# Optimization experiments

Measured on AMD Instinct MI355X. Metric: run time of the kernel, lower is better.

Reference implementation:

```python
import jax, jax.numpy as jnp
import numpy as np

GRID_SHAPE = (128, 128, 128, 8)
N_POINTS = 2_000_000


def setup_inputs() -> dict:
    key = jax.random.key(0)
    k1, k2 = jax.random.split(key)
    coords = jax.random.uniform(k1, (N_POINTS, 3), dtype=jnp.float32)
    grid = jax.random.normal(k2, GRID_SHAPE, dtype=jnp.float32)
    bbox_min = jnp.zeros((3,), dtype=jnp.float32)
    bbox_max = jnp.ones((3,), dtype=jnp.float32)
    return {"coords": coords, "grid": grid, "bbox_min": bbox_min, "bbox_max": bbox_max}


def reference(coords, grid, bbox_min, bbox_max):
    # coords: [N, 3]; grid: [X, Y, Z, C]
    eps = 1e-06
    coords = coords[:, :3]
    scale = jnp.maximum(bbox_max - bbox_min, eps)
    normalized = jnp.clip((coords - bbox_min) / scale, 0.0, 1.0)
    grid_size = jnp.asarray(grid.shape[:3], dtype=jnp.int64)  # [3]
    pos = normalized * (grid_size.astype(coords.dtype) - 1.0)  # [N, 3]
    idx0 = jnp.floor(pos).astype(jnp.int64)                    # [N, 3]
    idx1 = jnp.minimum(idx0 + 1, grid_size - 1)                # [N, 3]
    weight = jnp.clip(pos - idx0.astype(coords.dtype), 0.0, 1.0)  # [N, 3]

    x0, y0, z0 = idx0[:, 0], idx0[:, 1], idx0[:, 2]
    x1, y1, z1 = idx1[:, 0], idx1[:, 1], idx1[:, 2]
    wx, wy, wz = weight[:, 0:1], weight[:, 1:2], weight[:, 2:3]  # each [N, 1]

    c000 = grid[x0, y0, z0]
    c100 = grid[x1, y0, z0]
    c010 = grid[x0, y1, z0]
    c110 = grid[x1, y1, z0]
    c001 = grid[x0, y0, z1]
    c101 = grid[x1, y0, z1]
    c011 = grid[x0, y1, z1]
    c111 = grid[x1, y1, z1]

    c00 = c000 * (1.0 - wx) + c100 * wx
    c01 = c001 * (1.0 - wx) + c101 * wx
    c10 = c010 * (1.0 - wx) + c110 * wx
    c11 = c011 * (1.0 - wx) + c111 * wx
    c0 = c00 * (1.0 - wy) + c10 * wy
    c1 = c01 * (1.0 - wy) + c11 * wy
    return c0 * (1.0 - wz) + c1 * wz  # [N, C]
```

## Files before the change

kernel.cpp:

```cpp
#include <hip/hip_runtime.h>


#define GS    128
#define NBX   32
#define NB2   2048
#define CAP1  65536
#define CAP2  1280
#define K_PTS 1024

__device__ __forceinline__ void cell_of(
    float cx, float cy, float cz,
    float b0x, float b0y, float b0z,
    float sx, float sy, float sz,
    int& x0, int& y0, int& z0)
{
    float nx = fminf(fmaxf((cx - b0x) / sx, 0.0f), 1.0f);
    float ny = fminf(fmaxf((cy - b0y) / sy, 0.0f), 1.0f);
    float nz = fminf(fmaxf((cz - b0z) / sz, 0.0f), 1.0f);
    x0 = (int)(nx * (float)(GS - 1));
    y0 = (int)(ny * (float)(GS - 1));
    z0 = (int)(nz * (float)(GS - 1));
}

__global__ __launch_bounds__(256) void k_init(
    unsigned* __restrict__ cursor32, unsigned* __restrict__ cursor2048)
{
    int i = blockIdx.x * 256 + threadIdx.x;
    if (i < NBX) cursor32[i] = (unsigned)i * CAP1;
    if (i < NB2) cursor2048[i] = (unsigned)i * CAP2;
}

__global__ __launch_bounds__(256) void k_scatter1(
    const float* __restrict__ coords,
    const float* __restrict__ bbox_min,
    const float* __restrict__ bbox_max,
    unsigned* __restrict__ cursor32,
    float4* __restrict__ recs1, int n)
{
    __shared__ float4 srec[K_PTS];
    __shared__ unsigned char sbkt[K_PTS];
    __shared__ unsigned cnt[NBX], lbase[NBX], gbase[NBX];

    int t = threadIdx.x;
    if (t < NBX) cnt[t] = 0;
    __syncthreads();

    float b0x = bbox_min[0];
    float sx  = fmaxf(bbox_max[0] - b0x, 1e-6f);
    long long base = (long long)blockIdx.x * K_PTS;
    int m = (int)min((long long)K_PTS, (long long)n - base);

    float cx[4], cy[4], cz[4];
    int bb[4]; unsigned rr[4];
    int j0 = 4 * t;
    if (j0 + 3 < m) {
        const float4* c4 = (const float4*)coords + (size_t)blockIdx.x * 768 + 3 * t;
        float4 f0 = c4[0], f1 = c4[1], f2 = c4[2];
        cx[0] = f0.x; cy[0] = f0.y; cz[0] = f0.z;
        cx[1] = f0.w; cy[1] = f1.x; cz[1] = f1.y;
        cx[2] = f1.z; cy[2] = f1.w; cz[2] = f2.x;
        cx[3] = f2.y; cy[3] = f2.z; cz[3] = f2.w;
    } else {
#pragma unroll
        for (int p = 0; p < 4; ++p) {
            int j = j0 + p;
            if (j < m) {
                long long i = base + j;
                cx[p] = coords[3 * i]; cy[p] = coords[3 * i + 1]; cz[p] = coords[3 * i + 2];
            }
        }
    }
#pragma unroll
    for (int p = 0; p < 4; ++p) {
        int j = j0 + p;
        if (j < m) {
            float nx = fminf(fmaxf((cx[p] - b0x) / sx, 0.0f), 1.0f);
            bb[p] = ((int)(nx * (float)(GS - 1))) >> 2;
            rr[p] = atomicAdd(&cnt[bb[p]], 1u);
        }
    }
    __syncthreads();

    if (t == 0) {
        unsigned acc = 0;
        for (int j = 0; j < NBX; ++j) { lbase[j] = acc; acc += cnt[j]; }
    }
    if (t < NBX && cnt[t]) gbase[t] = atomicAdd(&cursor32[t], cnt[t]);
    __syncthreads();

#pragma unroll
    for (int p = 0; p < 4; ++p) {
        int j = j0 + p;
        if (j < m) {
            unsigned slot = lbase[bb[p]] + rr[p];
            float4 r; r.x = cx[p]; r.y = cy[p]; r.z = cz[p];
            r.w = __uint_as_float((unsigned)(base + j));
            srec[slot] = r;
            sbkt[slot] = (unsigned char)bb[p];
        }
    }
    __syncthreads();

#pragma unroll
    for (int k = 0; k < 4; ++k) {
        int j = k * 256 + t;
        if (j < m) {
            int b = sbkt[j];
            unsigned d = gbase[b] + (unsigned)j - lbase[b];
            if (d < (unsigned)(b + 1) * CAP1) recs1[d] = srec[j];
        }
    }
}

__global__ __launch_bounds__(256) void k_scatter2(
    const float4* __restrict__ recs1,
    const float* __restrict__ bbox_min,
    const float* __restrict__ bbox_max,
    const unsigned* __restrict__ cursor32_final,
    unsigned* __restrict__ cursor2048,
    float4* __restrict__ recs2)
{
    __shared__ float4 srec[K_PTS];
    __shared__ unsigned char sbkt[K_PTS];
    __shared__ unsigned cnt[64], lbase[64], gbase[64];

    int s = blockIdx.x >> 6;
    int c = blockIdx.x & 63;
    unsigned fill = cursor32_final[s] - (unsigned)s * CAP1;
    if (fill > CAP1) fill = CAP1;
    unsigned off = (unsigned)c * 1024;
    if (off >= fill) return;
    int m = (int)min(1024u, fill - off);

    int t = threadIdx.x;
    if (t < 64) cnt[t] = 0;
    __syncthreads();

    float b0x = bbox_min[0], b0y = bbox_min[1], b0z = bbox_min[2];
    float sx = fmaxf(bbox_max[0] - b0x, 1e-6f);
    float sy = fmaxf(bbox_max[1] - b0y, 1e-6f);
    float sz = fmaxf(bbox_max[2] - b0z, 1e-6f);
    long long base = (long long)s * CAP1 + off;

    float4 rc[4]; int bb[4]; unsigned rr[4];
#pragma unroll
    for (int k = 0; k < 4; ++k) {
        int j = k * 256 + t;
        if (j < m) {
            rc[k] = recs1[base + j];
            int x0, y0, z0;
            cell_of(rc[k].x, rc[k].y, rc[k].z, b0x, b0y, b0z, sx, sy, sz, x0, y0, z0);
            bb[k] = ((y0 >> 2) << 1) | (z0 >> 6);
            rr[k] = atomicAdd(&cnt[bb[k]], 1u);
        }
    }
    __syncthreads();

    if (t == 0) {
        unsigned acc = 0;
        for (int j = 0; j < 64; ++j) { lbase[j] = acc; acc += cnt[j]; }
    }
    if (t < 64 && cnt[t]) gbase[t] = atomicAdd(&cursor2048[s * 64 + t], cnt[t]);
    __syncthreads();

#pragma unroll
    for (int k = 0; k < 4; ++k) {
        int j = k * 256 + t;
        if (j < m) {
            unsigned slot = lbase[bb[k]] + rr[k];
            srec[slot] = rc[k];
            sbkt[slot] = (unsigned char)bb[k];
        }
    }
    __syncthreads();

#pragma unroll
    for (int k = 0; k < 4; ++k) {
        int j = k * 256 + t;
        if (j < m) {
            int lb = sbkt[j];
            unsigned g = (unsigned)s * 64 + lb;
            unsigned d = gbase[lb] + (unsigned)j - lbase[lb];
            if (d < (g + 1) * CAP2) recs2[d] = srec[j];
        }
    }
}

#define LDS_CELLS (5 * 5 * 65)
__global__ __launch_bounds__(256) void k_interp_staged(
    const float4* __restrict__ recs2,
    const unsigned* __restrict__ cursor2048_final,
    const float* __restrict__ grid,
    const float* __restrict__ bbox_min,
    const float* __restrict__ bbox_max,
    float4* __restrict__ out4)
{
    __shared__ float4 tile[LDS_CELLS * 2];

    int ob = blockIdx.x;
    int b  = (ob & 7) * 256 + (ob >> 3);

    unsigned s0 = (unsigned)b * CAP2;
    unsigned e  = cursor2048_final[b];
    unsigned cap_end = s0 + CAP2;
    if (e > cap_end) e = cap_end;
    if (e <= s0) return;

    int xs = b >> 6, ys = (b >> 1) & 31, zh = b & 1;
    int t = threadIdx.x;

    const float4* g4 = (const float4*)grid;
    for (int k = t; k < LDS_CELLS * 2; k += 256) {
        int c  = k >> 1, half = k & 1;
        int lx = c / 325;
        int r2 = c - lx * 325;
        int ly = r2 / 65;
        int lz = r2 - ly * 65;
        int gx = min(xs * 4 + lx, GS - 1);
        int gy = min(ys * 4 + ly, GS - 1);
        int gz = min(zh * 64 + lz, GS - 1);
        tile[k] = g4[(((gx * GS) + gy) * GS + gz) * 2 + half];
    }
    __syncthreads();

    const float eps = 1e-6f;
    float b0x = bbox_min[0], b0y = bbox_min[1], b0z = bbox_min[2];
    float sx = fmaxf(bbox_max[0] - b0x, eps);
    float sy = fmaxf(bbox_max[1] - b0y, eps);
    float sz = fmaxf(bbox_max[2] - b0z, eps);

    int pair = t >> 1, half = t & 1;

    for (unsigned cb = s0; cb < e; cb += 128) {
        unsigned j = cb + pair;
        if (j >= e) continue;
        float4 rec = recs2[j];
        unsigned orig = __float_as_uint(rec.w);

        float nx = fminf(fmaxf((rec.x - b0x) / sx, 0.0f), 1.0f);
        float ny = fminf(fmaxf((rec.y - b0y) / sy, 0.0f), 1.0f);
        float nz = fminf(fmaxf((rec.z - b0z) / sz, 0.0f), 1.0f);
        float px = nx * (float)(GS - 1);
        float py = ny * (float)(GS - 1);
        float pz = nz * (float)(GS - 1);
        int x0 = (int)px, y0 = (int)py, z0 = (int)pz;
        int x1 = min(x0 + 1, GS - 1);
        int y1 = min(y0 + 1, GS - 1);
        int z1 = min(z0 + 1, GS - 1);
        float wx = fminf(fmaxf(px - (float)x0, 0.0f), 1.0f);
        float wy = fminf(fmaxf(py - (float)y0, 0.0f), 1.0f);
        float wz = fminf(fmaxf(pz - (float)z0, 0.0f), 1.0f);

        int lx0 = x0 - xs * 4, lx1 = x1 - xs * 4;
        int ly0 = y0 - ys * 4, ly1 = y1 - ys * 4;
        int lz0 = z0 - zh * 64, lz1 = z1 - zh * 64;

        int c000 = ((lx0 * 5 + ly0) * 65 + lz0) * 2 + half;
        int c100 = ((lx1 * 5 + ly0) * 65 + lz0) * 2 + half;
        int c010 = ((lx0 * 5 + ly1) * 65 + lz0) * 2 + half;
        int c110 = ((lx1 * 5 + ly1) * 65 + lz0) * 2 + half;
        int c001 = ((lx0 * 5 + ly0) * 65 + lz1) * 2 + half;
        int c101 = ((lx1 * 5 + ly0) * 65 + lz1) * 2 + half;
        int c011 = ((lx0 * 5 + ly1) * 65 + lz1) * 2 + half;
        int c111 = ((lx1 * 5 + ly1) * 65 + lz1) * 2 + half;

        float ux = 1.0f - wx, uy = 1.0f - wy, uz = 1.0f - wz;
        float w000 = ux*uy*uz, w100 = wx*uy*uz, w010 = ux*wy*uz, w110 = wx*wy*uz;
        float w001 = ux*uy*wz, w101 = wx*uy*wz, w011 = ux*wy*wz, w111 = wx*wy*wz;

        float4 A = tile[c000], B = tile[c100], C = tile[c010], D = tile[c110];
        float4 E = tile[c001], F = tile[c101], H = tile[c011], Kk = tile[c111];

        float4 o;
        o.x = A.x*w000 + B.x*w100 + C.x*w010 + D.x*w110 + E.x*w001 + F.x*w101 + H.x*w011 + Kk.x*w111;
        o.y = A.y*w000 + B.y*w100 + C.y*w010 + D.y*w110 + E.y*w001 + F.y*w101 + H.y*w011 + Kk.y*w111;
        o.z = A.z*w000 + B.z*w100 + C.z*w010 + D.z*w110 + E.z*w001 + F.z*w101 + H.z*w011 + Kk.z*w111;
        o.w = A.w*w000 + B.w*w100 + C.w*w010 + D.w*w110 + E.w*w001 + F.w*w101 + H.w*w011 + Kk.w*w111;

        out4[(long long)orig * 2 + half] = o;
    }
}

__global__ __launch_bounds__(256) void trilerp_direct(
    const float* __restrict__ coords,
    const float* __restrict__ grid,
    const float* __restrict__ bbox_min,
    const float* __restrict__ bbox_max,
    float* __restrict__ out, int n)
{
    int i = blockIdx.x * blockDim.x + threadIdx.x;
    if (i >= n) return;
    const float eps = 1e-6f;
    float b0x = bbox_min[0], b0y = bbox_min[1], b0z = bbox_min[2];
    float sx = fmaxf(bbox_max[0] - b0x, eps);
    float sy = fmaxf(bbox_max[1] - b0y, eps);
    float sz = fmaxf(bbox_max[2] - b0z, eps);
    float nx = fminf(fmaxf((coords[3*i] - b0x) / sx, 0.0f), 1.0f);
    float ny = fminf(fmaxf((coords[3*i+1] - b0y) / sy, 0.0f), 1.0f);
    float nz = fminf(fmaxf((coords[3*i+2] - b0z) / sz, 0.0f), 1.0f);
    float px = nx * (float)(GS - 1), py = ny * (float)(GS - 1), pz = nz * (float)(GS - 1);
    int x0 = (int)px, y0 = (int)py, z0 = (int)pz;
    int x1 = min(x0 + 1, GS - 1), y1 = min(y0 + 1, GS - 1), z1 = min(z0 + 1, GS - 1);
    float wx = fminf(fmaxf(px - (float)x0, 0.0f), 1.0f);
    float wy = fminf(fmaxf(py - (float)y0, 0.0f), 1.0f);
    float wz = fminf(fmaxf(pz - (float)z0, 0.0f), 1.0f);
    float ux = 1.0f - wx, uy = 1.0f - wy, uz = 1.0f - wz;
    float w000 = ux*uy*uz, w100 = wx*uy*uz, w010 = ux*wy*uz, w110 = wx*wy*uz;
    float w001 = ux*uy*wz, w101 = wx*uy*wz, w011 = ux*wy*wz, w111 = wx*wy*wz;
    const float4* g4 = (const float4*)grid;
    int bx0 = x0 * GS, bx1 = x1 * GS;
    int p000 = ((bx0 + y0) * GS + z0) * 2, p100 = ((bx1 + y0) * GS + z0) * 2;
    int p010 = ((bx0 + y1) * GS + z0) * 2, p110 = ((bx1 + y1) * GS + z0) * 2;
    int p001 = ((bx0 + y0) * GS + z1) * 2, p101 = ((bx1 + y0) * GS + z1) * 2;
    int p011 = ((bx0 + y1) * GS + z1) * 2, p111 = ((bx1 + y1) * GS + z1) * 2;
    float4 a0 = g4[p000], a1 = g4[p000+1], b0 = g4[p100], b1 = g4[p100+1];
    float4 c0 = g4[p010], c1 = g4[p010+1], d0 = g4[p110], d1 = g4[p110+1];
    float4 e0 = g4[p001], e1 = g4[p001+1], f0 = g4[p101], f1 = g4[p101+1];
    float4 h0 = g4[p011], h1 = g4[p011+1], k0 = g4[p111], k1 = g4[p111+1];
    float4 o0, o1;
    o0.x = a0.x*w000 + b0.x*w100 + c0.x*w010 + d0.x*w110 + e0.x*w001 + f0.x*w101 + h0.x*w011 + k0.x*w111;
    o0.y = a0.y*w000 + b0.y*w100 + c0.y*w010 + d0.y*w110 + e0.y*w001 + f0.y*w101 + h0.y*w011 + k0.y*w111;
    o0.z = a0.z*w000 + b0.z*w100 + c0.z*w010 + d0.z*w110 + e0.z*w001 + f0.z*w101 + h0.z*w011 + k0.z*w111;
    o0.w = a0.w*w000 + b0.w*w100 + c0.w*w010 + d0.w*w110 + e0.w*w001 + f0.w*w101 + h0.w*w011 + k0.w*w111;
    o1.x = a1.x*w000 + b1.x*w100 + c1.x*w010 + d1.x*w110 + e1.x*w001 + f1.x*w101 + h1.x*w011 + k1.x*w111;
    o1.y = a1.y*w000 + b1.y*w100 + c1.y*w010 + d1.y*w110 + e1.y*w001 + f1.y*w101 + h1.y*w011 + k1.y*w111;
    o1.z = a1.z*w000 + b1.z*w100 + c1.z*w010 + d1.z*w110 + e1.z*w001 + f1.z*w101 + h1.z*w011 + k1.z*w111;
    o1.w = a1.w*w000 + b1.w*w100 + c1.w*w010 + d1.w*w110 + e1.w*w001 + f1.w*w101 + h1.w*w011 + k1.w*w111;
    float4* outp = (float4*)out;
    outp[(long long)i * 2 + 0] = o0;
    outp[(long long)i * 2 + 1] = o1;
}

extern "C" void kernel_launch(void* const* d_in, const int* in_sizes, int n_in,
                              void* d_out, int out_size, void* d_ws, size_t ws_size,
                              hipStream_t stream) {
    const float* coords   = (const float*)d_in[0];
    const float* grid     = (const float*)d_in[1];
    const float* bbox_min = (const float*)d_in[2];
    const float* bbox_max = (const float*)d_in[3];
    float* out = (float*)d_out;

    int n = in_sizes[0] / 3;

    size_t cur32_off = 0;
    size_t cur2_off  = 256;
    size_t recs1_off = 16384;
    size_t recs2_off = recs1_off + (size_t)NBX * CAP1 * 16;
    size_t needed    = recs2_off + (size_t)NB2 * CAP2 * 16;

    int nb_sort = (n + K_PTS - 1) / K_PTS;
    int nb_dir  = (n + 255) / 256;

    if (ws_size >= needed) {
        unsigned* cur32 = (unsigned*)((char*)d_ws + cur32_off);
        unsigned* cur2  = (unsigned*)((char*)d_ws + cur2_off);
        float4*   recs1 = (float4*)((char*)d_ws + recs1_off);
        float4*   recs2 = (float4*)((char*)d_ws + recs2_off);

        k_init    <<<8, 256, 0, stream>>>(cur32, cur2);
        k_scatter1<<<nb_sort, 256, 0, stream>>>(coords, bbox_min, bbox_max, cur32, recs1, n);
        k_scatter2<<<NBX * 64, 256, 0, stream>>>(recs1, bbox_min, bbox_max, cur32, cur2, recs2);
        k_interp_staged<<<NB2, 256, 0, stream>>>(recs2, cur2, grid, bbox_min, bbox_max,
                                                 (float4*)out);
    } else {
        trilerp_direct<<<nb_dir, 256, 0, stream>>>(coords, grid, bbox_min, bbox_max, out, n);
    }
}
```

Baseline: 98.24 us.

## Halve z extent of interpolation tiles, double bucket count, stage records in LDS

Second-level buckets now split z into quarters (32 cells) instead of halves, which doubles the bucket count to 4096 and shrinks the per-bucket grid tile to 5x5x33 cells. The interpolation kernel now runs 512 threads per block and first copies its bucket's point records into shared memory before working on them. The smaller tile means less redundant grid halo loading per point and more, smaller blocks to spread across the GPU. The risk is that the per-bucket capacity of 704 is tight against the expected ~488 points per bucket, so a heavily filled bucket could overflow and drop points.

```diff
diff --git a/kernel.cpp b/kernel.cpp
--- a/kernel.cpp
+++ b/kernel.cpp
@@ -3,10 +3,11 @@
 
 #define GS    128
 #define NBX   32
-#define NB2   2048
+#define NB2   4096
 #define CAP1  65536
-#define CAP2  1280
+#define CAP2  704
 #define K_PTS 1024
+#define HCELLS (5 * 5 * 33)
 
 __device__ __forceinline__ void cell_of(
     float cx, float cy, float cz,
@@ -23,11 +24,11 @@
 }
 
 __global__ __launch_bounds__(256) void k_init(
-    unsigned* __restrict__ cursor32, unsigned* __restrict__ cursor2048)
+    unsigned* __restrict__ cursor32, unsigned* __restrict__ cursor4096)
 {
     int i = blockIdx.x * 256 + threadIdx.x;
     if (i < NBX) cursor32[i] = (unsigned)i * CAP1;
-    if (i < NB2) cursor2048[i] = (unsigned)i * CAP2;
+    if (i < NB2) cursor4096[i] = (unsigned)i * CAP2;
 }
 
 __global__ __launch_bounds__(256) void k_scatter1(
@@ -117,12 +118,12 @@
     const float* __restrict__ bbox_min,
     const float* __restrict__ bbox_max,
     const unsigned* __restrict__ cursor32_final,
-    unsigned* __restrict__ cursor2048,
+    unsigned* __restrict__ cursor4096,
     float4* __restrict__ recs2)
 {
     __shared__ float4 srec[K_PTS];
     __shared__ unsigned char sbkt[K_PTS];
-    __shared__ unsigned cnt[64], lbase[64], gbase[64];
+    __shared__ unsigned cnt[128], lbase[128], gbase[128];
 
     int s = blockIdx.x >> 6;
     int c = blockIdx.x & 63;
@@ -133,7 +134,7 @@
     int m = (int)min(1024u, fill - off);
 
     int t = threadIdx.x;
-    if (t < 64) cnt[t] = 0;
+    if (t < 128) cnt[t] = 0;
     __syncthreads();
 
     float b0x = bbox_min[0], b0y = bbox_min[1], b0z = bbox_min[2];
@@ -150,7 +151,7 @@
             rc[k] = recs1[base + j];
             int x0, y0, z0;
             cell_of(rc[k].x, rc[k].y, rc[k].z, b0x, b0y, b0z, sx, sy, sz, x0, y0, z0);
-            bb[k] = ((y0 >> 2) << 1) | (z0 >> 6);
+            bb[k] = ((y0 >> 2) << 2) | (z0 >> 5);
             rr[k] = atomicAdd(&cnt[bb[k]], 1u);
         }
     }
@@ -158,9 +159,9 @@
 
     if (t == 0) {
         unsigned acc = 0;
-        for (int j = 0; j < 64; ++j) { lbase[j] = acc; acc += cnt[j]; }
-    }
-    if (t < 64 && cnt[t]) gbase[t] = atomicAdd(&cursor2048[s * 64 + t], cnt[t]);
+        for (int j = 0; j < 128; ++j) { lbase[j] = acc; acc += cnt[j]; }
+    }
+    if (t < 128 && cnt[t]) gbase[t] = atomicAdd(&cursor4096[s * 128 + t], cnt[t]);
     __syncthreads();
 
 #pragma unroll
@@ -179,46 +180,49 @@
         int j = k * 256 + t;
         if (j < m) {
             int lb = sbkt[j];
-            unsigned g = (unsigned)s * 64 + lb;
+            unsigned g = (unsigned)s * 128 + lb;
             unsigned d = gbase[lb] + (unsigned)j - lbase[lb];
             if (d < (g + 1) * CAP2) recs2[d] = srec[j];
         }
     }
 }
 
-#define LDS_CELLS (5 * 5 * 65)
-__global__ __launch_bounds__(256) void k_interp_staged(
+__global__ __launch_bounds__(512) void k_interp_staged(
     const float4* __restrict__ recs2,
-    const unsigned* __restrict__ cursor2048_final,
+    const unsigned* __restrict__ cursor4096_final,
     const float* __restrict__ grid,
     const float* __restrict__ bbox_min,
     const float* __restrict__ bbox_max,
     float4* __restrict__ out4)
 {
-    __shared__ float4 tile[LDS_CELLS * 2];
+    __shared__ float4 tile[HCELLS * 2];
+    __shared__ float4 srec[CAP2];
 
     int ob = blockIdx.x;
-    int b  = (ob & 7) * 256 + (ob >> 3);
+    int b  = (ob & 7) * 512 + (ob >> 3);
 
     unsigned s0 = (unsigned)b * CAP2;
-    unsigned e  = cursor2048_final[b];
+    unsigned e  = cursor4096_final[b];
     unsigned cap_end = s0 + CAP2;
     if (e > cap_end) e = cap_end;
     if (e <= s0) return;
-
-    int xs = b >> 6, ys = (b >> 1) & 31, zh = b & 1;
+    int cnt = (int)(e - s0);
+
+    int xs = b >> 7, ys = (b >> 2) & 31, zq = b & 3;
     int t = threadIdx.x;
 
+    for (int k = t; k < cnt; k += 512) srec[k] = recs2[s0 + k];
+
     const float4* g4 = (const float4*)grid;
-    for (int k = t; k < LDS_CELLS * 2; k += 256) {
+    for (int k = t; k < HCELLS * 2; k += 512) {
         int c  = k >> 1, half = k & 1;
-        int lx = c / 325;
-        int r2 = c - lx * 325;
-        int ly = r2 / 65;
-        int lz = r2 - ly * 65;
+        int lx = c / 165;
+        int r2 = c - lx * 165;
+        int ly = r2 / 33;
+        int lz = r2 - ly * 33;
         int gx = min(xs * 4 + lx, GS - 1);
         int gy = min(ys * 4 + ly, GS - 1);
-        int gz = min(zh * 64 + lz, GS - 1);
+        int gz = min(zq * 32 + lz, GS - 1);
         tile[k] = g4[(((gx * GS) + gy) * GS + gz) * 2 + half];
     }
     __syncthreads();
@@ -231,10 +235,10 @@
 
     int pair = t >> 1, half = t & 1;
 
-    for (unsigned cb = s0; cb < e; cb += 128) {
-        unsigned j = cb + pair;
-        if (j >= e) continue;
-        float4 rec = recs2[j];
+    for (int cb = 0; cb < cnt; cb += 256) {
+        int j = cb + pair;
+        if (j >= cnt) continue;
+        float4 rec = srec[j];
         unsigned orig = __float_as_uint(rec.w);
 
         float nx = fminf(fmaxf((rec.x - b0x) / sx, 0.0f), 1.0f);
@@ -253,16 +257,16 @@
 
         int lx0 = x0 - xs * 4, lx1 = x1 - xs * 4;
         int ly0 = y0 - ys * 4, ly1 = y1 - ys * 4;
-        int lz0 = z0 - zh * 64, lz1 = z1 - zh * 64;
-
-        int c000 = ((lx0 * 5 + ly0) * 65 + lz0) * 2 + half;
-        int c100 = ((lx1 * 5 + ly0) * 65 + lz0) * 2 + half;
-        int c010 = ((lx0 * 5 + ly1) * 65 + lz0) * 2 + half;
-        int c110 = ((lx1 * 5 + ly1) * 65 + lz0) * 2 + half;
-        int c001 = ((lx0 * 5 + ly0) * 65 + lz1) * 2 + half;
-        int c101 = ((lx1 * 5 + ly0) * 65 + lz1) * 2 + half;
-        int c011 = ((lx0 * 5 + ly1) * 65 + lz1) * 2 + half;
-        int c111 = ((lx1 * 5 + ly1) * 65 + lz1) * 2 + half;
+        int lz0 = z0 - zq * 32, lz1 = z1 - zq * 32;
+
+        int c000 = ((lx0 * 5 + ly0) * 33 + lz0) * 2 + half;
+        int c100 = ((lx1 * 5 + ly0) * 33 + lz0) * 2 + half;
+        int c010 = ((lx0 * 5 + ly1) * 33 + lz0) * 2 + half;
+        int c110 = ((lx1 * 5 + ly1) * 33 + lz0) * 2 + half;
+        int c001 = ((lx0 * 5 + ly0) * 33 + lz1) * 2 + half;
+        int c101 = ((lx1 * 5 + ly0) * 33 + lz1) * 2 + half;
+        int c011 = ((lx0 * 5 + ly1) * 33 + lz1) * 2 + half;
+        int c111 = ((lx1 * 5 + ly1) * 33 + lz1) * 2 + half;
 
         float ux = 1.0f - wx, uy = 1.0f - wy, uz = 1.0f - wz;
         float w000 = ux*uy*uz, w100 = wx*uy*uz, w010 = ux*wy*uz, w110 = wx*wy*uz;
@@ -344,7 +348,7 @@
 
     size_t cur32_off = 0;
     size_t cur2_off  = 256;
-    size_t recs1_off = 16384;
+    size_t recs1_off = 32768;
     size_t recs2_off = recs1_off + (size_t)NBX * CAP1 * 16;
     size_t needed    = recs2_off + (size_t)NB2 * CAP2 * 16;
 
@@ -357,10 +361,10 @@
         float4*   recs1 = (float4*)((char*)d_ws + recs1_off);
         float4*   recs2 = (float4*)((char*)d_ws + recs2_off);
 
-        k_init    <<<8, 256, 0, stream>>>(cur32, cur2);
+        k_init    <<<16, 256, 0, stream>>>(cur32, cur2);
         k_scatter1<<<nb_sort, 256, 0, stream>>>(coords, bbox_min, bbox_max, cur32, recs1, n);
         k_scatter2<<<NBX * 64, 256, 0, stream>>>(recs1, bbox_min, bbox_max, cur32, cur2, recs2);
-        k_interp_staged<<<NB2, 256, 0, stream>>>(recs2, cur2, grid, bbox_min, bbox_max,
+        k_interp_staged<<<NB2, 512, 0, stream>>>(recs2, cur2, grid, bbox_min, bbox_max,
                                                  (float4*)out);
     } else {
         trilerp_direct<<<nb_dir, 256, 0, stream>>>(coords, grid, bbox_min, bbox_max, out, n);
```

Measured after the change: 94.41 us (median of 2 runs). 3.9% less time.
